# Kernel optimization log

Measured on AMD Instinct MI355X. Metric: run time of the kernel, lower is better.

## Reference

```python
import jax, jax.numpy as jnp
import numpy as np

WIN = 256  # window_size from init_kwargs


def _stream_attn(q, k, v, win, hollow):
    """Banded sliding-window attention.

    hollow=False (s-stream): key j attended iff 0 <= i - j < win (last `win` tokens incl. self).
    hollow=True  (c-stream): key j attended iff win <= i - j < 2*win (tokens [i-2W+1, i-W]).
    Returns (out [B,S,H,D], lse [B,H,S]) with lse = -inf for fully-masked rows.
    """
    B, S, H, D = q.shape
    nb = S // win
    scale = D ** -0.5
    qb = q.reshape(B, nb, win, H, D)
    kb = k.reshape(B, nb, win, H, D)
    vb = v.reshape(B, nb, win, H, D)
    pad = ((0, 0), (2, 0), (0, 0), (0, 0), (0, 0))
    kp = jnp.pad(kb, pad)
    vp = jnp.pad(vb, pad)
    k_ctx = jnp.concatenate([kp[:, t:t + nb] for t in range(3)], axis=2)  # [B,nb,3W,H,D]
    v_ctx = jnp.concatenate([vp[:, t:t + nb] for t in range(3)], axis=2)
    lq = jnp.arange(win)[:, None]
    kk = jnp.arange(3 * win)[None, :]
    t_blk = kk // win
    lk = kk % win
    rel = (2 - t_blk) * win + lq - lk  # i - j, shape [W, 3W]
    if hollow:
        wmask = (rel >= win) & (rel < 2 * win)
    else:
        wmask = (rel >= 0) & (rel < win)
    blk_ok = (jnp.arange(nb)[:, None] - 2 + (jnp.arange(3 * win) // win)[None, :]) >= 0  # [nb,3W]
    mask = wmask[None] & blk_ok[:, None, :]  # [nb, W, 3W]
    logits = jnp.einsum('bnqhd,bnkhd->bnhqk', qb, k_ctx) * scale  # [B,nb,H,W,3W]
    logits = jnp.where(mask[None, :, None], logits, -jnp.inf)
    m = jnp.max(logits, axis=-1)  # [B,nb,H,W]
    ms = jnp.where(jnp.isneginf(m), 0.0, m)
    p = jnp.exp(logits - ms[..., None])
    denom = jnp.sum(p, axis=-1)  # [B,nb,H,W]
    out = jnp.einsum('bnhqk,bnkhd->bnqhd', p, v_ctx)  # [B,nb,W,H,D]
    safe = jnp.where(denom > 0, denom, 1.0)
    out = out / jnp.moveaxis(safe, 2, 3)[..., None]
    lse = jnp.where(denom > 0, jnp.log(safe) + m, -jnp.inf)  # [B,nb,H,W]
    out = out.reshape(B, S, H, D)
    lse = jnp.moveaxis(lse, 1, 2).reshape(B, H, S)
    return out, lse


def _merge(out_c, lse_c, out_s, lse_s):
    # faithful jax version of merge_attn_states_torch (LSE online-softmax merge)
    m = jnp.maximum(lse_c, lse_s)
    ms = jnp.where(jnp.isneginf(m), 0.0, m)
    ec = jnp.exp(lse_c - ms)
    es = jnp.exp(lse_s - ms)
    se = ec + es  # s-stream always has >=1 key (self), so se > 0
    c_scale = jnp.moveaxis(ec / se, 1, 2)[..., None]  # [B,S,H,1]
    s_scale = jnp.moveaxis(es / se, 1, 2)[..., None]
    return out_c * c_scale + out_s * s_scale


def setup_inputs() -> dict:
    key = jax.random.key(0)
    k1, k2, k3 = jax.random.split(key, 3)
    B, S, H, D = 2, 2048, 16, 128
    return {
        'query': jax.random.normal(k1, (B, S, H, D), dtype=jnp.float32),
        'key': jax.random.normal(k2, (B, S, H, D), dtype=jnp.float32),
        'value': jax.random.normal(k3, (B, S, H, D), dtype=jnp.float32),
    }


def reference(query, key, value):
    out_c, lse_c = _stream_attn(query, key, value, WIN, hollow=True)   # c-stream: [i-2W, i-W]
    out_s, lse_s = _stream_attn(query, key, value, WIN, hollow=False)  # s-stream: last W tokens
    return _merge(out_c, lse_c, out_s, lse_s)
```

## Files before the change

kernel.cpp:

```cpp
#include <hip/hip_runtime.h>
#include <math.h>

#define S_LEN 2048
#define NH    16
#define DD    128
#define SROW  (NH*DD)
#define WIN2  512
#define BQ    128
#define BK    64
#define RSQ   136
#define RS    72

typedef __bf16 bf16x8 __attribute__((ext_vector_type(8)));
typedef __bf16 bf16x4 __attribute__((ext_vector_type(4)));
typedef float  f32x4  __attribute__((ext_vector_type(4)));

__device__ __forceinline__ f32x4 mfma16(bf16x8 a, bf16x8 b, f32x4 c) {
    return __builtin_amdgcn_mfma_f32_16x16x32_bf16(a, b, c, 0, 0, 0);
}

__device__ __forceinline__ unsigned int pack_bf16(float lo, float hi) {
    return (unsigned int)__builtin_bit_cast(unsigned short, (__bf16)lo)
         | ((unsigned int)__builtin_bit_cast(unsigned short, (__bf16)hi) << 16);
}

#define OFF_VT 8704
#define OFF_P  17920
#define SMEM_ELEMS 27136

__global__ __launch_bounds__(512, 4)
void swattn_kernel(const float* __restrict__ Qg, const float* __restrict__ Kg,
                   const float* __restrict__ Vg, float* __restrict__ Og) {
    __shared__ __align__(16) __bf16 smem[SMEM_ELEMS];

    const int t   = threadIdx.x;
    const int w   = t >> 6;
    const int l   = t & 63;
    const int r16 = l & 15;
    const int g4  = l >> 4;
    const int Qlo = blockIdx.x * BQ;
    const int h   = blockIdx.y;
    const int b   = blockIdx.z;

    const size_t bh = ((size_t)b * S_LEN) * SROW + (size_t)h * DD;
    const float C1 = 0.08838834764831845f * 1.44269504088896340f;

    for (int it = 0; it < 8; ++it) {
        int f   = it * 512 + t;
        int q_l = f >> 5;
        int dq  = (f & 31) * 4;
        const float4 v = *(const float4*)&Qg[bh + (size_t)(Qlo + q_l) * SROW + dq];
        bf16x4 o4 = { (__bf16)(v.x * C1), (__bf16)(v.y * C1),
                      (__bf16)(v.z * C1), (__bf16)(v.w * C1) };
        *(bf16x4*)&smem[q_l * RSQ + dq] = o4;
    }
    __syncthreads();

    bf16x8 qf[4];
#pragma unroll
    for (int sl = 0; sl < 4; ++sl)
        qf[sl] = *(const bf16x8*)&smem[(w*16 + r16) * RSQ + sl*32 + g4*8];
    __syncthreads();

    const f32x4 zero4 = {0.f, 0.f, 0.f, 0.f};
    f32x4 oacc[8];
#pragma unroll
    for (int dg = 0; dg < 8; ++dg) oacc[dg] = zero4;
    float m_run = -1e4f;
    float l_run = 0.f;

    const int q_w = Qlo + w * 16;
    const int gv = l >> 5;
    const int rv = l & 31;

    int cb = Qlo - (WIN2 - 1);
    if (cb < 0) cb = 0;
    cb &= ~(BK - 1);
    const int Qhi = Qlo + BQ - 1;

    for (int c0 = cb; c0 <= Qhi; c0 += BK) {
        for (int it = 0; it < 4; ++it) {
            int f   = it * 512 + t;
            int k_l = f >> 5;
            int dq  = (f & 31) * 4;
            const float4 v = *(const float4*)&Kg[bh + (size_t)(c0 + k_l) * SROW + dq];
            bf16x4 o4 = { (__bf16)v.x, (__bf16)v.y, (__bf16)v.z, (__bf16)v.w };
            *(bf16x4*)&smem[k_l * RSQ + dq] = o4;
        }
        for (int it = 0; it < 4; ++it) {
            int k0l = w * 8 + it * 2;
            const float4 v4 = *(const float4*)&Vg[bh + (size_t)(c0 + k0l + gv) * SROW + 4*rv];
            float ox = __shfl_xor(v4.x, 32);
            float oy = __shfl_xor(v4.y, 32);
            float oz = __shfl_xor(v4.z, 32);
            float ow = __shfl_xor(v4.w, 32);
            float lo0, hi0, lo1, hi1; int d0;
            if (gv == 0) { lo0 = v4.x; hi0 = ox;   lo1 = v4.y; hi1 = oy;   d0 = 4*rv; }
            else         { lo0 = oz;   hi0 = v4.z; lo1 = ow;   hi1 = v4.w; d0 = 4*rv + 2; }
            int col = k0l ^ ((rv & 7) << 3);
            *(unsigned int*)&smem[OFF_VT + (d0    ) * RS + col] = pack_bf16(lo0, hi0);
            *(unsigned int*)&smem[OFF_VT + (d0 + 1) * RS + col] = pack_bf16(lo1, hi1);
        }
        __syncthreads();

        const bool act = (q_w + 15 >= c0) && (q_w <= c0 + (BK - 1) + (WIN2 - 1));
        if (act) {
            f32x4 st[4] = { zero4, zero4, zero4, zero4 };
#pragma unroll
            for (int sl = 0; sl < 4; ++sl)
#pragma unroll
                for (int kg = 0; kg < 4; ++kg) {
                    bf16x8 kf = *(const bf16x8*)&smem[(kg*16 + r16) * RSQ + sl*32 + g4*8];
                    st[kg] = mfma16(kf, qf[sl], st[kg]);
                }

            const bool fv = (q_w >= c0 + (BK - 1)) && (q_w + 15 <= c0 + (WIN2 - 1));
            if (!fv) {
                int iq = q_w + r16;
#pragma unroll
                for (int kg = 0; kg < 4; ++kg) {
                    int relb = iq - (c0 + kg*16 + 4*g4);
#pragma unroll
                    for (int rg = 0; rg < 4; ++rg) {
                        bool ok = ((unsigned)(relb - rg)) < (unsigned)WIN2;
                        st[kg][rg] = ok ? st[kg][rg] : -1e30f;
                    }
                }
            }

            float mc = -1e30f;
#pragma unroll
            for (int kg = 0; kg < 4; ++kg)
#pragma unroll
                for (int rg = 0; rg < 4; ++rg) mc = fmaxf(mc, st[kg][rg]);
            mc = fmaxf(mc, __shfl_xor(mc, 16));
            mc = fmaxf(mc, __shfl_xor(mc, 32));
            float mn = fmaxf(m_run, mc);
            float alpha = exp2f(m_run - mn);
            m_run = mn;
            float sum = 0.f;
#pragma unroll
            for (int kg = 0; kg < 4; ++kg)
#pragma unroll
                for (int rg = 0; rg < 4; ++rg) {
                    float p = exp2f(st[kg][rg] - mn);
                    st[kg][rg] = p;
                    sum += p;
                }
            sum += __shfl_xor(sum, 16);
            sum += __shfl_xor(sum, 32);
            l_run = l_run * alpha + sum;

#pragma unroll
            for (int kg = 0; kg < 4; ++kg) {
                f32x4 pv = st[kg];
                bf16x4 p4 = { (__bf16)pv[0], (__bf16)pv[1], (__bf16)pv[2], (__bf16)pv[3] };
                *(bf16x4*)&smem[OFF_P + (w*16 + r16) * RS + kg*16 + 4*g4] = p4;
            }

#pragma unroll
            for (int dg = 0; dg < 8; ++dg)
#pragma unroll
                for (int rg = 0; rg < 4; ++rg) oacc[dg][rg] *= alpha;

#pragma unroll
            for (int ks = 0; ks < 2; ++ks) {
                bf16x8 pf = *(const bf16x8*)&smem[OFF_P + (w*16 + r16) * RS + ks*32 + g4*8];
#pragma unroll
                for (int dg = 0; dg < 8; ++dg) {
                    int col = (ks*32 + g4*8) ^ (32*(dg&1) + 8*(r16>>2));
                    bf16x8 vf = *(const bf16x8*)&smem[OFF_VT + (dg*16 + r16) * RS + col];
                    oacc[dg] = mfma16(vf, pf, oacc[dg]);
                }
            }
        }
        __syncthreads();
    }

    float inv = 1.f / l_run;
    int q = q_w + r16;
    size_t base = bh + (size_t)q * SROW;
#pragma unroll
    for (int dg = 0; dg < 8; ++dg) {
        f32x4 o = oacc[dg];
        float4 res = { o[0]*inv, o[1]*inv, o[2]*inv, o[3]*inv };
        *(float4*)&Og[base + dg*16 + 4*g4] = res;
    }
}

extern "C" void kernel_launch(void* const* d_in, const int* in_sizes, int n_in,
                              void* d_out, int out_size, void* d_ws, size_t ws_size,
                              hipStream_t stream) {
    const float* q = (const float*)d_in[0];
    const float* k = (const float*)d_in[1];
    const float* v = (const float*)d_in[2];
    float* o = (float*)d_out;
    int B = in_sizes[0] / (S_LEN * NH * DD);
    dim3 grid(S_LEN / BQ, NH, B);
    swattn_kernel<<<grid, 512, 0, stream>>>(q, k, v, o);
}
```

Measured before the change: 174.8 us.

## Prefetch next K/V tile into registers and change V-transpose LDS swizzle

Global loads of the next K and V tile are issued into registers right after the barrier, so they overlap the QK^T, softmax and PV compute of the current tile. The first tile's loads are also issued before the Q staging. The V^T shared-memory layout switches from an XOR swizzle to a rotation-style swizzle, and the PV loop reads each fragment as two 4-element halves to avoid bank conflicts. This adds 32 prefetch registers per thread, which could pressure occupancy under launch bounds (512, 4), and it turns each 128-bit LDS read into two 64-bit reads.

```diff
diff --git a/kernel.cpp b/kernel.cpp
--- a/kernel.cpp
+++ b/kernel.cpp
@@ -44,6 +44,55 @@
 
     const size_t bh = ((size_t)b * S_LEN) * SROW + (size_t)h * DD;
     const float C1 = 0.08838834764831845f * 1.44269504088896340f;
+
+    const int kst_row = t >> 5;
+    const int kst_col = (t & 31) * 4;
+    const int gv = l >> 5;
+    const int rv = l & 31;
+
+    float4 kpre[4], vpre[4];
+
+    auto issue_loads = [&](int c0) {
+#pragma unroll
+        for (int it = 0; it < 4; ++it)
+            kpre[it] = *(const float4*)&Kg[bh + (size_t)(c0 + it*16 + kst_row) * SROW + kst_col];
+#pragma unroll
+        for (int it = 0; it < 4; ++it) {
+            int k0l = w * 8 + it * 2;
+            vpre[it] = *(const float4*)&Vg[bh + (size_t)(c0 + k0l + gv) * SROW + 4*rv];
+        }
+    };
+
+    auto write_stage = [&]() {
+#pragma unroll
+        for (int it = 0; it < 4; ++it) {
+            const float4 v = kpre[it];
+            bf16x4 o4 = { (__bf16)v.x, (__bf16)v.y, (__bf16)v.z, (__bf16)v.w };
+            *(bf16x4*)&smem[(it*16 + kst_row) * RSQ + kst_col] = o4;
+        }
+#pragma unroll
+        for (int it = 0; it < 4; ++it) {
+            int k0l = w * 8 + it * 2;
+            const float4 v4 = vpre[it];
+            float ox = __shfl_xor(v4.x, 32);
+            float oy = __shfl_xor(v4.y, 32);
+            float oz = __shfl_xor(v4.z, 32);
+            float ow = __shfl_xor(v4.w, 32);
+            float lo0, hi0, lo1, hi1; int d0;
+            if (gv == 0) { lo0 = v4.x; hi0 = ox;   lo1 = v4.y; hi1 = oy;   d0 = 4*rv; }
+            else         { lo0 = oz;   hi0 = v4.z; lo1 = ow;   hi1 = v4.w; d0 = 4*rv + 2; }
+            int col = (k0l + 4*(rv & 15)) & 63;
+            *(unsigned int*)&smem[OFF_VT + (d0    ) * RS + col] = pack_bf16(lo0, hi0);
+            *(unsigned int*)&smem[OFF_VT + (d0 + 1) * RS + col] = pack_bf16(lo1, hi1);
+        }
+    };
+
+    int cb = Qlo - (WIN2 - 1);
+    if (cb < 0) cb = 0;
+    cb &= ~(BK - 1);
+    const int Qhi = Qlo + BQ - 1;
+
+    issue_loads(cb);
 
     for (int it = 0; it < 8; ++it) {
         int f   = it * 512 + t;
@@ -70,38 +119,12 @@
     float l_run = 0.f;
 
     const int q_w = Qlo + w * 16;
-    const int gv = l >> 5;
-    const int rv = l & 31;
-
-    int cb = Qlo - (WIN2 - 1);
-    if (cb < 0) cb = 0;
-    cb &= ~(BK - 1);
-    const int Qhi = Qlo + BQ - 1;
 
     for (int c0 = cb; c0 <= Qhi; c0 += BK) {
-        for (int it = 0; it < 4; ++it) {
-            int f   = it * 512 + t;
-            int k_l = f >> 5;
-            int dq  = (f & 31) * 4;
-            const float4 v = *(const float4*)&Kg[bh + (size_t)(c0 + k_l) * SROW + dq];
-            bf16x4 o4 = { (__bf16)v.x, (__bf16)v.y, (__bf16)v.z, (__bf16)v.w };
-            *(bf16x4*)&smem[k_l * RSQ + dq] = o4;
-        }
-        for (int it = 0; it < 4; ++it) {
-            int k0l = w * 8 + it * 2;
-            const float4 v4 = *(const float4*)&Vg[bh + (size_t)(c0 + k0l + gv) * SROW + 4*rv];
-            float ox = __shfl_xor(v4.x, 32);
-            float oy = __shfl_xor(v4.y, 32);
-            float oz = __shfl_xor(v4.z, 32);
-            float ow = __shfl_xor(v4.w, 32);
-            float lo0, hi0, lo1, hi1; int d0;
-            if (gv == 0) { lo0 = v4.x; hi0 = ox;   lo1 = v4.y; hi1 = oy;   d0 = 4*rv; }
-            else         { lo0 = oz;   hi0 = v4.z; lo1 = ow;   hi1 = v4.w; d0 = 4*rv + 2; }
-            int col = k0l ^ ((rv & 7) << 3);
-            *(unsigned int*)&smem[OFF_VT + (d0    ) * RS + col] = pack_bf16(lo0, hi0);
-            *(unsigned int*)&smem[OFF_VT + (d0 + 1) * RS + col] = pack_bf16(lo1, hi1);
-        }
+        write_stage();
         __syncthreads();
+
+        if (c0 + BK <= Qhi) issue_loads(c0 + BK);
 
         const bool act = (q_w + 15 >= c0) && (q_w <= c0 + (BK - 1) + (WIN2 - 1));
         if (act) {
@@ -168,8 +191,12 @@
                 bf16x8 pf = *(const bf16x8*)&smem[OFF_P + (w*16 + r16) * RS + ks*32 + g4*8];
 #pragma unroll
                 for (int dg = 0; dg < 8; ++dg) {
-                    int col = (ks*32 + g4*8) ^ (32*(dg&1) + 8*(r16>>2));
-                    bf16x8 vf = *(const bf16x8*)&smem[OFF_VT + (dg*16 + r16) * RS + col];
+                    int d   = dg*16 + r16;
+                    int s_e = ks*32 + g4*8 + 4*((4*dg + (r16 >> 2)) & 15);
+                    const __bf16* row = &smem[OFF_VT + d * RS];
+                    bf16x4 vlo = *(const bf16x4*)&row[s_e & 63];
+                    bf16x4 vhi = *(const bf16x4*)&row[(s_e + 4) & 63];
+                    bf16x8 vf = __builtin_shufflevector(vlo, vhi, 0,1,2,3,4,5,6,7);
                     oacc[dg] = mfma16(vf, pf, oacc[dg]);
                 }
             }
```

Result: slower. 225.2 us (+28.8%).
